# Kernel tuning notes

Hardware: AMD Instinct MI355X
Metric: run time of the kernel (lower is better)

Reference implementation:

```python
import jax, jax.numpy as jnp
import numpy as np

THRESHOLD = 0.5
EPS = 1e-8


def cos_sim(a, b):
    # a: [M, D], b: [N, D] -> [M, N] cosine similarity
    a_n = jnp.linalg.norm(a, axis=1, keepdims=True)
    b_n = jnp.linalg.norm(b, axis=1, keepdims=True)
    a_norm = a / jnp.maximum(a_n, EPS)
    b_norm = b / jnp.maximum(b_n, EPS)
    return a_norm @ b_norm.T


def setup_inputs() -> dict:
    key = jax.random.key(0)
    k1, k2, k3, k4 = jax.random.split(key, 4)
    N1, N2, FEA_FT, W_FT = 8192, 8192, 128, 64
    fea1 = jax.random.normal(k1, (N1, FEA_FT), dtype=jnp.float32)
    fea2 = jax.random.normal(k2, (N2, FEA_FT), dtype=jnp.float32)
    # xavier_uniform with relu gain sqrt(2): limit = gain * sqrt(6/(fan_in+fan_out))
    gain = float(np.sqrt(2.0))
    limit = gain * float(np.sqrt(6.0 / (FEA_FT + W_FT)))
    w1 = jax.random.uniform(k3, (FEA_FT, W_FT), minval=-limit, maxval=limit, dtype=jnp.float32)
    w2 = jax.random.uniform(k4, (FEA_FT, W_FT), minval=-limit, maxval=limit, dtype=jnp.float32)
    return {"fea1": fea1, "fea2": fea2, "w1": w1, "w2": w2}


def reference(fea1, fea2, w1, w2):
    embed1 = fea1 @ w1  # [N1, w_ft]
    embed2 = fea2 @ w2  # [N2, w_ft]
    sim_up = cos_sim(embed1, embed2)  # [N1, N2]
    sims_up = jnp.where(sim_up < THRESHOLD, jnp.zeros_like(sim_up), sim_up)
    sim_uu = cos_sim(embed1, embed1)  # [N1, N1]
    sims_uu = jnp.where(sim_uu < THRESHOLD, jnp.zeros_like(sim_uu), sim_uu)
    # Edge lists in the original are nonzero(sims_up)/nonzero(sims_uu); we return
    # the thresholded similarity matrices (jit-safe, fixed shape), stacked.
    return jnp.stack([sims_up, sims_uu], axis=0)  # [2, N, N]
```

## Files before the change

### kernel.cpp

```cpp
#include <hip/hip_runtime.h>

#define THRESH 0.5f
#define BAND   1e-3f

constexpr int N  = 8192;
constexpr int FD = 128;
constexpr int WD = 64;
constexpr unsigned FIX_CAP = 16u << 20;

typedef __attribute__((ext_vector_type(8)))  short short8;
typedef __attribute__((ext_vector_type(4)))  float f32x4;

static __device__ __forceinline__ unsigned short f2bf(float x) {
  union { float f; unsigned u; } v; v.f = x;
  unsigned r = v.u + 0x7FFFu + ((v.u >> 16) & 1u);
  return (unsigned short)(r >> 16);
}
static __device__ __forceinline__ float bf2f(unsigned short h) {
  union { unsigned u; float f; } v; v.u = (unsigned)h << 16;
  return v.f;
}

__global__ __launch_bounds__(256) void embed_norm(
    const float* __restrict__ fea1, const float* __restrict__ fea2,
    const float* __restrict__ w1,   const float* __restrict__ w2,
    float* __restrict__ E1n, float* __restrict__ E2n,
    unsigned short* __restrict__ E1h, unsigned short* __restrict__ E1l,
    unsigned short* __restrict__ E2h, unsigned short* __restrict__ E2l,
    unsigned* __restrict__ fix_cnt) {
  if (blockIdx.x == 0 && blockIdx.y == 0 && threadIdx.x == 0) *fix_cnt = 0;

  const int which = blockIdx.y;
  const float* __restrict__ fea = which ? fea2 : fea1;
  const float* __restrict__ w   = which ? w2   : w1;
  float*          En = which ? E2n : E1n;
  unsigned short* Eh = which ? E2h : E1h;
  unsigned short* El = which ? E2l : E1l;

  __shared__ float wl[FD * WD];
  __shared__ float fl[32][FD];

  const int t    = threadIdx.x;
  const int row0 = blockIdx.x * 32;

#pragma unroll
  for (int i = 0; i < 8; ++i) {
    const int idx = (t + i * 256) * 4;
    *(float4*)&wl[idx] = *(const float4*)&w[idx];
  }
#pragma unroll
  for (int i = 0; i < 4; ++i) {
    const int idx = t + i * 256;
    const int r = idx >> 5;
    const int c = (idx & 31) * 4;
    *(float4*)&fl[r][c] = *(const float4*)&fea[(size_t)(row0 + r) * FD + c];
  }
  __syncthreads();

  const int wave = t >> 6, lane = t & 63;
#pragma unroll 1
  for (int rr = 0; rr < 8; ++rr) {
    const int r = wave * 8 + rr;
    float acc = 0.f;
#pragma unroll 16
    for (int k = 0; k < FD; ++k)
      acc = fmaf(fl[r][k], wl[k * WD + lane], acc);
    float ss = acc * acc;
#pragma unroll
    for (int m = 32; m >= 1; m >>= 1) ss += __shfl_xor(ss, m, 64);
    const float scale = 1.f / fmaxf(sqrtf(ss), 1e-8f);
    const float e = acc * scale;
    const size_t o = (size_t)(row0 + r) * WD + lane;
    En[o] = e;
    const unsigned short h = f2bf(e);
    Eh[o] = h;
    El[o] = f2bf(e - bf2f(h));
  }
}

__global__ __launch_bounds__(256) void sim_mfma(
    const unsigned short* __restrict__ E1h, const unsigned short* __restrict__ E1l,
    const unsigned short* __restrict__ E2h, const unsigned short* __restrict__ E2l,
    float* __restrict__ out,
    unsigned* __restrict__ fix_cnt, unsigned* __restrict__ fix_lst) {
  const int bi = blockIdx.y, bj = blockIdx.x;
  const int t = threadIdx.x, w = t >> 6, lane = t & 63;
  const int wr = w >> 1, wc = w & 1;
  const int row0 = bi * 128 + wr * 64;
  const int col0 = bj * 128 + wc * 64;
  const int fr = lane & 15;
  const int fg = lane >> 4;

#pragma unroll 1
  for (int plane = 0; plane < 2; ++plane) {
    const unsigned short* __restrict__ Bh = plane ? E1h : E2h;
    const unsigned short* __restrict__ Bl = plane ? E1l : E2l;

    f32x4 acc[4][4] = {};
#pragma unroll
    for (int ks = 0; ks < 2; ++ks) {
      const int koff = ks * 32 + fg * 8;
      short8 ah[4], al[4], bh[4], bl[4];
#pragma unroll
      for (int ti = 0; ti < 4; ++ti) {
        const size_t ra = (size_t)(row0 + ti * 16 + fr) * WD + koff;
        ah[ti] = *(const short8*)(E1h + ra);
        al[ti] = *(const short8*)(E1l + ra);
        const size_t rb = (size_t)(col0 + ti * 16 + fr) * WD + koff;
        bh[ti] = *(const short8*)(Bh + rb);
        bl[ti] = *(const short8*)(Bl + rb);
      }
#pragma unroll
      for (int ti = 0; ti < 4; ++ti)
#pragma unroll
        for (int tj = 0; tj < 4; ++tj) {
          acc[ti][tj] = __builtin_amdgcn_mfma_f32_16x16x32_bf16(ah[ti], bh[tj], acc[ti][tj], 0, 0, 0);
          acc[ti][tj] = __builtin_amdgcn_mfma_f32_16x16x32_bf16(ah[ti], bl[tj], acc[ti][tj], 0, 0, 0);
          acc[ti][tj] = __builtin_amdgcn_mfma_f32_16x16x32_bf16(al[ti], bh[tj], acc[ti][tj], 0, 0, 0);
          acc[ti][tj] = __builtin_amdgcn_mfma_f32_16x16x32_bf16(al[ti], bl[tj], acc[ti][tj], 0, 0, 0);
        }
    }

    float* __restrict__ o = out + (size_t)plane * N * N;
#pragma unroll
    for (int ti = 0; ti < 4; ++ti)
#pragma unroll
      for (int tj = 0; tj < 4; ++tj)
#pragma unroll
        for (int r = 0; r < 4; ++r) {
          const int R = row0 + ti * 16 + fg * 4 + r;
          const int C = col0 + tj * 16 + fr;
          const float v = acc[ti][tj][r];
          if (fabsf(v - THRESH) < BAND) {
            const unsigned idx = atomicAdd(fix_cnt, 1u);
            if (idx < FIX_CAP)
              fix_lst[idx] = ((unsigned)plane << 26) | ((unsigned)R << 13) | (unsigned)C;
          }
          o[(size_t)R * N + C] = (v < THRESH) ? 0.f : v;
        }
  }
}

__global__ __launch_bounds__(256) void fixup(
    const float* __restrict__ E1, const float* __restrict__ E2,
    float* __restrict__ out,
    const unsigned* __restrict__ fix_cnt, const unsigned* __restrict__ fix_lst) {
  unsigned n = *fix_cnt;
  if (n > FIX_CAP) n = FIX_CAP;
  for (unsigned idx = blockIdx.x * blockDim.x + threadIdx.x; idx < n;
       idx += gridDim.x * blockDim.x) {
    const unsigned e = fix_lst[idx];
    const int plane = (int)(e >> 26);
    const int i = (int)((e >> 13) & 8191);
    const int j = (int)(e & 8191);
    const float* __restrict__ B = plane ? E1 : E2;
    float s = 0.f;
#pragma unroll 16
    for (int k = 0; k < WD; ++k)
      s = fmaf(E1[i * WD + k], B[j * WD + k], s);
    out[(size_t)plane * N * N + (size_t)i * N + j] = (s < THRESH) ? 0.f : s;
  }
}

extern "C" void kernel_launch(void* const* d_in, const int* in_sizes, int n_in,
                              void* d_out, int out_size, void* d_ws, size_t ws_size,
                              hipStream_t stream) {
  const float* fea1 = (const float*)d_in[0];
  const float* fea2 = (const float*)d_in[1];
  const float* w1   = (const float*)d_in[2];
  const float* w2   = (const float*)d_in[3];
  float* out = (float*)d_out;

  char* ws = (char*)d_ws;
  float*          E1n = (float*)(ws);
  float*          E2n = (float*)(ws + (2u << 20));
  unsigned short* E1h = (unsigned short*)(ws + (4u << 20));
  unsigned short* E1l = (unsigned short*)(ws + (5u << 20));
  unsigned short* E2h = (unsigned short*)(ws + (6u << 20));
  unsigned short* E2l = (unsigned short*)(ws + (7u << 20));
  unsigned*   fix_cnt = (unsigned*)(ws + (8u << 20));
  unsigned*   fix_lst = (unsigned*)(ws + (8u << 20) + 256);

  embed_norm<<<dim3(N / 32, 2), 256, 0, stream>>>(
      fea1, fea2, w1, w2, E1n, E2n, E1h, E1l, E2h, E2l, fix_cnt);
  sim_mfma<<<dim3(64, 64), 256, 0, stream>>>(
      E1h, E1l, E2h, E2l, out, fix_cnt, fix_lst);
  fixup<<<64, 256, 0, stream>>>(E1n, E2n, out, fix_cnt, fix_lst);
}
```

Before: 641.9 us.

## Swap MFMA operands for row-contiguous float4 nontemporal stores and inline fixup

Swaps the MFMA operand order so each lane holds four consecutive output columns of one row. The output can then be written as 16-byte nontemporal stores instead of scattered scalar stores. Near-threshold entries are recomputed inline in fp32 through a noinline dot-product helper, which removes the atomic fix list and the separate fixup kernel. The E1 fragments are hoisted out of the plane loop so they are loaded once. The cost is possible divergence from the inline exact dot product inside the store loop.

```diff
diff --git a/kernel.cpp b/kernel.cpp
--- a/kernel.cpp
+++ b/kernel.cpp
@@ -6,7 +6,6 @@
 constexpr int N  = 8192;
 constexpr int FD = 128;
 constexpr int WD = 64;
-constexpr unsigned FIX_CAP = 16u << 20;
 
 typedef __attribute__((ext_vector_type(8)))  short short8;
 typedef __attribute__((ext_vector_type(4)))  float f32x4;
@@ -21,15 +20,20 @@
   return v.f;
 }
 
+static __device__ __noinline__ float exact_dot(const float* __restrict__ a,
+                                               const float* __restrict__ b) {
+  float s = 0.f;
+#pragma unroll 1
+  for (int k = 0; k < WD; ++k) s = fmaf(a[k], b[k], s);
+  return s;
+}
+
 __global__ __launch_bounds__(256) void embed_norm(
     const float* __restrict__ fea1, const float* __restrict__ fea2,
     const float* __restrict__ w1,   const float* __restrict__ w2,
     float* __restrict__ E1n, float* __restrict__ E2n,
     unsigned short* __restrict__ E1h, unsigned short* __restrict__ E1l,
-    unsigned short* __restrict__ E2h, unsigned short* __restrict__ E2l,
-    unsigned* __restrict__ fix_cnt) {
-  if (blockIdx.x == 0 && blockIdx.y == 0 && threadIdx.x == 0) *fix_cnt = 0;
-
+    unsigned short* __restrict__ E2h, unsigned short* __restrict__ E2l) {
   const int which = blockIdx.y;
   const float* __restrict__ fea = which ? fea2 : fea1;
   const float* __restrict__ w   = which ? w2   : w1;
@@ -81,8 +85,8 @@
 __global__ __launch_bounds__(256) void sim_mfma(
     const unsigned short* __restrict__ E1h, const unsigned short* __restrict__ E1l,
     const unsigned short* __restrict__ E2h, const unsigned short* __restrict__ E2l,
-    float* __restrict__ out,
-    unsigned* __restrict__ fix_cnt, unsigned* __restrict__ fix_lst) {
+    const float* __restrict__ E1n, const float* __restrict__ E2n,
+    float* __restrict__ out) {
   const int bi = blockIdx.y, bj = blockIdx.x;
   const int t = threadIdx.x, w = t >> 6, lane = t & 63;
   const int wr = w >> 1, wc = w & 1;
@@ -91,74 +95,61 @@
   const int fr = lane & 15;
   const int fg = lane >> 4;
 
+  short8 yh[2][4], yl[2][4];
+#pragma unroll
+  for (int ks = 0; ks < 2; ++ks)
+#pragma unroll
+    for (int ti = 0; ti < 4; ++ti) {
+      const size_t r = (size_t)(row0 + ti * 16 + fr) * WD + ks * 32 + fg * 8;
+      yh[ks][ti] = *(const short8*)(E1h + r);
+      yl[ks][ti] = *(const short8*)(E1l + r);
+    }
+
 #pragma unroll 1
   for (int plane = 0; plane < 2; ++plane) {
-    const unsigned short* __restrict__ Bh = plane ? E1h : E2h;
-    const unsigned short* __restrict__ Bl = plane ? E1l : E2l;
+    const unsigned short* __restrict__ Xh = plane ? E1h : E2h;
+    const unsigned short* __restrict__ Xl = plane ? E1l : E2l;
+    const float*          __restrict__ Xn = plane ? E1n : E2n;
 
     f32x4 acc[4][4] = {};
 #pragma unroll
     for (int ks = 0; ks < 2; ++ks) {
-      const int koff = ks * 32 + fg * 8;
-      short8 ah[4], al[4], bh[4], bl[4];
+      short8 xh[4], xl[4];
 #pragma unroll
-      for (int ti = 0; ti < 4; ++ti) {
-        const size_t ra = (size_t)(row0 + ti * 16 + fr) * WD + koff;
-        ah[ti] = *(const short8*)(E1h + ra);
-        al[ti] = *(const short8*)(E1l + ra);
-        const size_t rb = (size_t)(col0 + ti * 16 + fr) * WD + koff;
-        bh[ti] = *(const short8*)(Bh + rb);
-        bl[ti] = *(const short8*)(Bl + rb);
+      for (int tj = 0; tj < 4; ++tj) {
+        const size_t r = (size_t)(col0 + tj * 16 + fr) * WD + ks * 32 + fg * 8;
+        xh[tj] = *(const short8*)(Xh + r);
+        xl[tj] = *(const short8*)(Xl + r);
       }
 #pragma unroll
-      for (int ti = 0; ti < 4; ++ti)
+      for (int tj = 0; tj < 4; ++tj)
 #pragma unroll
-        for (int tj = 0; tj < 4; ++tj) {
-          acc[ti][tj] = __builtin_amdgcn_mfma_f32_16x16x32_bf16(ah[ti], bh[tj], acc[ti][tj], 0, 0, 0);
-          acc[ti][tj] = __builtin_amdgcn_mfma_f32_16x16x32_bf16(ah[ti], bl[tj], acc[ti][tj], 0, 0, 0);
-          acc[ti][tj] = __builtin_amdgcn_mfma_f32_16x16x32_bf16(al[ti], bh[tj], acc[ti][tj], 0, 0, 0);
-          acc[ti][tj] = __builtin_amdgcn_mfma_f32_16x16x32_bf16(al[ti], bl[tj], acc[ti][tj], 0, 0, 0);
+        for (int ti = 0; ti < 4; ++ti) {
+          acc[tj][ti] = __builtin_amdgcn_mfma_f32_16x16x32_bf16(xh[tj], yh[ks][ti], acc[tj][ti], 0, 0, 0);
+          acc[tj][ti] = __builtin_amdgcn_mfma_f32_16x16x32_bf16(xh[tj], yl[ks][ti], acc[tj][ti], 0, 0, 0);
+          acc[tj][ti] = __builtin_amdgcn_mfma_f32_16x16x32_bf16(xl[tj], yh[ks][ti], acc[tj][ti], 0, 0, 0);
+          acc[tj][ti] = __builtin_amdgcn_mfma_f32_16x16x32_bf16(xl[tj], yl[ks][ti], acc[tj][ti], 0, 0, 0);
         }
     }
 
     float* __restrict__ o = out + (size_t)plane * N * N;
 #pragma unroll
-    for (int ti = 0; ti < 4; ++ti)
+    for (int tj = 0; tj < 4; ++tj)
 #pragma unroll
-      for (int tj = 0; tj < 4; ++tj)
+      for (int ti = 0; ti < 4; ++ti) {
+        const int m  = row0 + ti * 16 + fr;
+        const int nb = col0 + tj * 16 + fg * 4;
+        const f32x4 v = acc[tj][ti];
+        f32x4 sv;
 #pragma unroll
         for (int r = 0; r < 4; ++r) {
-          const int R = row0 + ti * 16 + fg * 4 + r;
-          const int C = col0 + tj * 16 + fr;
-          const float v = acc[ti][tj][r];
-          if (fabsf(v - THRESH) < BAND) {
-            const unsigned idx = atomicAdd(fix_cnt, 1u);
-            if (idx < FIX_CAP)
-              fix_lst[idx] = ((unsigned)plane << 26) | ((unsigned)R << 13) | (unsigned)C;
-          }
-          o[(size_t)R * N + C] = (v < THRESH) ? 0.f : v;
+          float val = v[r];
+          if (fabsf(val - THRESH) < BAND)
+            val = exact_dot(E1n + (size_t)m * WD, Xn + (size_t)(nb + r) * WD);
+          sv[r] = (val < THRESH) ? 0.f : val;
         }
-  }
-}
-
-__global__ __launch_bounds__(256) void fixup(
-    const float* __restrict__ E1, const float* __restrict__ E2,
-    float* __restrict__ out,
-    const unsigned* __restrict__ fix_cnt, const unsigned* __restrict__ fix_lst) {
-  unsigned n = *fix_cnt;
-  if (n > FIX_CAP) n = FIX_CAP;
-  for (unsigned idx = blockIdx.x * blockDim.x + threadIdx.x; idx < n;
-       idx += gridDim.x * blockDim.x) {
-    const unsigned e = fix_lst[idx];
-    const int plane = (int)(e >> 26);
-    const int i = (int)((e >> 13) & 8191);
-    const int j = (int)(e & 8191);
-    const float* __restrict__ B = plane ? E1 : E2;
-    float s = 0.f;
-#pragma unroll 16
-    for (int k = 0; k < WD; ++k)
-      s = fmaf(E1[i * WD + k], B[j * WD + k], s);
-    out[(size_t)plane * N * N + (size_t)i * N + j] = (s < THRESH) ? 0.f : s;
+        __builtin_nontemporal_store(sv, (f32x4*)(o + (size_t)m * N + nb));
+      }
   }
 }
 
@@ -178,12 +169,9 @@
   unsigned short* E1l = (unsigned short*)(ws + (5u << 20));
   unsigned short* E2h = (unsigned short*)(ws + (6u << 20));
   unsigned short* E2l = (unsigned short*)(ws + (7u << 20));
-  unsigned*   fix_cnt = (unsigned*)(ws + (8u << 20));
-  unsigned*   fix_lst = (unsigned*)(ws + (8u << 20) + 256);
 
   embed_norm<<<dim3(N / 32, 2), 256, 0, stream>>>(
-      fea1, fea2, w1, w2, E1n, E2n, E1h, E1l, E2h, E2l, fix_cnt);
+      fea1, fea2, w1, w2, E1n, E2n, E1h, E1l, E2h, E2l);
   sim_mfma<<<dim3(64, 64), 256, 0, stream>>>(
-      E1h, E1l, E2h, E2l, out, fix_cnt, fix_lst);
-  fixup<<<64, 256, 0, stream>>>(E1n, E2n, out, fix_cnt, fix_lst);
+      E1h, E1l, E2h, E2l, E1n, E2n, out);
 }
```

Result: faster. 618.8 us (-3.6%).
